# Kernel optimization log

Hardware: AMD Instinct MI355X
Metric: run time of the kernel (lower is better)

## Reference

```python
import jax, jax.numpy as jnp
import numpy as np

D_MODEL = 1024

def setup_inputs() -> dict:
    key = jax.random.key(0)
    ks = jax.random.split(key, 7)
    x = jax.random.normal(ks[0], (4, 2048, D_MODEL), dtype=jnp.float32)
    s = 1.0 / np.sqrt(D_MODEL)
    Wq = jax.random.uniform(ks[1], (D_MODEL, D_MODEL), jnp.float32, -s, s)
    bq = jax.random.uniform(ks[2], (D_MODEL,), jnp.float32, -s, s)
    Wk = jax.random.uniform(ks[3], (D_MODEL, D_MODEL), jnp.float32, -s, s)
    bk = jax.random.uniform(ks[4], (D_MODEL,), jnp.float32, -s, s)
    Wv = jax.random.uniform(ks[5], (D_MODEL, D_MODEL), jnp.float32, -s, s)
    bv = jax.random.uniform(ks[6], (D_MODEL,), jnp.float32, -s, s)
    return {"x": x, "Wq": Wq, "bq": bq, "Wk": Wk, "bk": bk, "Wv": Wv, "bv": bv}

def reference(x, Wq, bq, Wk, bk, Wv, bv):
    # x: [B, S, D]; Linear weights stored torch-style [out, in] -> y = x @ W.T + b
    B, S, D = x.shape
    q = jnp.einsum('bsd,ed->bse', x, Wq) + bq
    k = jnp.einsum('bsd,ed->bse', x, Wk) + bk
    v = jnp.einsum('bsd,ed->bse', x, Wv) + bv
    scores = jnp.einsum('bqd,bkd->bqk', q, k) / jnp.sqrt(jnp.float32(D))
    causal = jnp.tril(jnp.ones((S, S), dtype=bool))  # True = allowed
    scores = jnp.where(causal[None], scores, -jnp.inf)
    probs = jax.nn.softmax(scores, axis=-1)
    return jnp.einsum('bqk,bkd->bqd', probs, v)
```

## Files before the change

### kernel.cpp

```cpp
#include <hip/hip_runtime.h>
#include <hip/hip_bf16.h>
#include <stdint.h>
#include <math.h>

using bf16 = __hip_bfloat16;
typedef __bf16 bf16x8 __attribute__((ext_vector_type(8)));
typedef float  f32x4  __attribute__((ext_vector_type(4)));

#define AS1 __attribute__((address_space(1)))
#define AS3 __attribute__((address_space(3)))

__device__ __forceinline__ void async_cp16(const void* g, void* l) {
    __builtin_amdgcn_global_load_lds((const AS1 void*)g, (AS3 void*)l, 16, 0, 0);
}

__global__ __launch_bounds__(256, 2) void gemm_qkv(
    const bf16* __restrict__ xb,
    const bf16* __restrict__ Wqb, const bf16* __restrict__ Wkb, const bf16* __restrict__ Wvb,
    const float* __restrict__ bq, const float* __restrict__ bk, const float* __restrict__ bv,
    bf16* __restrict__ Qb, bf16* __restrict__ Kb, bf16* __restrict__ Vt)
{
    const int bn = blockIdx.x, bm = blockIdx.y;
    const int seg = bn >> 3, bn_loc = bn & 7;
    const bf16*  W    = seg == 0 ? Wqb : (seg == 1 ? Wkb : Wvb);
    const float* bias = seg == 0 ? bq  : (seg == 1 ? bk  : bv);

    __shared__ bf16 sA[128 * 64];
    __shared__ bf16 sB[128 * 64];

    const int tid  = threadIdx.x;
    const int wave = tid >> 6, lane = tid & 63;
    const int wm = (wave >> 1) * 64, wn = (wave & 1) * 64;
    const int quad = lane >> 4, r16 = lane & 15;

    const bf16* Ab = xb + (long)bm * 128 * 1024;
    const bf16* Bb = W  + (long)bn_loc * 128 * 1024;

    const int rl = lane >> 3;
    const int cb = (lane & 7) ^ rl;
    const bf16* gA = Ab + (long)(wave * 32 + rl) * 1024 + cb * 8;
    const bf16* gB = Bb + (long)(wave * 32 + rl) * 1024 + cb * 8;
    char* lA = (char*)sA + wave * 32 * 128;
    char* lB = (char*)sB + wave * 32 * 128;

    f32x4 acc[4][4];
    const f32x4 zero = {0.f, 0.f, 0.f, 0.f};
#pragma unroll
    for (int i = 0; i < 4; i++)
#pragma unroll
        for (int j = 0; j < 4; j++) acc[i][j] = zero;

    for (int k0 = 0; k0 < 1024; k0 += 64) {
#pragma unroll
        for (int c = 0; c < 4; c++) {
            async_cp16(gA + (long)c * 8 * 1024 + k0, lA + c * 1024);
            async_cp16(gB + (long)c * 8 * 1024 + k0, lB + c * 1024);
        }
        __syncthreads();
#pragma unroll
        for (int kk = 0; kk < 2; kk++) {
            bf16x8 af[4], bfr[4];
#pragma unroll
            for (int t = 0; t < 4; t++) {
                int row  = wm + t * 16 + r16;
                int slot = (kk * 4 + quad) ^ (row & 7);
                af[t] = *(const bf16x8*)((const char*)sA + row * 128 + slot * 16);
            }
#pragma unroll
            for (int t = 0; t < 4; t++) {
                int row  = wn + t * 16 + r16;
                int slot = (kk * 4 + quad) ^ (row & 7);
                bfr[t] = *(const bf16x8*)((const char*)sB + row * 128 + slot * 16);
            }
#pragma unroll
            for (int mt = 0; mt < 4; mt++)
#pragma unroll
                for (int nt = 0; nt < 4; nt++)
                    acc[mt][nt] = __builtin_amdgcn_mfma_f32_16x16x32_bf16(
                        af[mt], bfr[nt], acc[mt][nt], 0, 0, 0);
        }
        __syncthreads();
    }

    bf16* O = seg == 0 ? Qb : Kb;
#pragma unroll
    for (int mt = 0; mt < 4; mt++) {
#pragma unroll
        for (int nt = 0; nt < 4; nt++) {
            int col = bn_loc * 128 + wn + nt * 16 + r16;
            float badd = bias[col];
#pragma unroll
            for (int rg = 0; rg < 4; rg++) {
                long token = (long)bm * 128 + wm + mt * 16 + quad * 4 + rg;
                bf16 v = __float2bfloat16(acc[mt][nt][rg] + badd);
                if (seg < 2) O[token * 1024 + col] = v;
                else         Vt[(long)col * 8192 + token] = v;
            }
        }
    }
}

__global__ __launch_bounds__(256, 2) void gemm_scores(
    const bf16* __restrict__ Qb, const bf16* __restrict__ Kb,
    bf16* __restrict__ P, float* __restrict__ spart)
{
    const int t = blockIdx.x, bz = blockIdx.z;
    int bm = (int)((sqrtf(8.f * t + 1.f) - 1.f) * 0.5f);
    while ((bm + 1) * (bm + 2) / 2 <= t) bm++;
    while (bm * (bm + 1) / 2 > t) bm--;
    const int bn = t - bm * (bm + 1) / 2;
    const bool diag = (bn == bm);

    __shared__ bf16 sA[128 * 64];
    __shared__ bf16 sB[128 * 64];

    const int tid  = threadIdx.x;
    const int wave = tid >> 6, lane = tid & 63;
    const int wm = (wave >> 1) * 64, wn = (wave & 1) * 64;
    const int quad = lane >> 4, r16 = lane & 15;
    const int half = wave & 1;

    const bf16* Ab = Qb + (long)bz * 2048 * 1024 + (long)bm * 128 * 1024;
    const bf16* Bb = Kb + (long)bz * 2048 * 1024 + (long)bn * 128 * 1024;

    const int rl = lane >> 3;
    const int cb = (lane & 7) ^ rl;
    const bf16* gA = Ab + (long)(wave * 32 + rl) * 1024 + cb * 8;
    const bf16* gB = Bb + (long)(wave * 32 + rl) * 1024 + cb * 8;
    char* lA = (char*)sA + wave * 32 * 128;
    char* lB = (char*)sB + wave * 32 * 128;

    f32x4 acc[4][4];
    const f32x4 zero = {0.f, 0.f, 0.f, 0.f};
#pragma unroll
    for (int i = 0; i < 4; i++)
#pragma unroll
        for (int j = 0; j < 4; j++) acc[i][j] = zero;

    for (int k0 = 0; k0 < 1024; k0 += 64) {
#pragma unroll
        for (int c = 0; c < 4; c++) {
            async_cp16(gA + (long)c * 8 * 1024 + k0, lA + c * 1024);
            async_cp16(gB + (long)c * 8 * 1024 + k0, lB + c * 1024);
        }
        __syncthreads();
#pragma unroll
        for (int kk = 0; kk < 2; kk++) {
            bf16x8 af[4], bfr[4];
#pragma unroll
            for (int t2 = 0; t2 < 4; t2++) {
                int row  = wm + t2 * 16 + r16;
                int slot = (kk * 4 + quad) ^ (row & 7);
                af[t2] = *(const bf16x8*)((const char*)sA + row * 128 + slot * 16);
            }
#pragma unroll
            for (int t2 = 0; t2 < 4; t2++) {
                int row  = wn + t2 * 16 + r16;
                int slot = (kk * 4 + quad) ^ (row & 7);
                bfr[t2] = *(const bf16x8*)((const char*)sB + row * 128 + slot * 16);
            }
#pragma unroll
            for (int mt = 0; mt < 4; mt++)
#pragma unroll
                for (int nt = 0; nt < 4; nt++)
                    acc[mt][nt] = __builtin_amdgcn_mfma_f32_16x16x32_bf16(
                        af[mt], bfr[nt], acc[mt][nt], 0, 0, 0);
        }
        __syncthreads();
    }

    bf16* Pb = P + (long)bz * 2048 * 2048 + (long)bm * 128 * 2048 + bn * 128;
    float rowsum[4][4];
#pragma unroll
    for (int mt = 0; mt < 4; mt++)
#pragma unroll
        for (int rg = 0; rg < 4; rg++) rowsum[mt][rg] = 0.f;

#pragma unroll
    for (int mt = 0; mt < 4; mt++) {
#pragma unroll
        for (int nt = 0; nt < 4; nt++) {
            int rcol = wn + nt * 16 + r16;
#pragma unroll
            for (int rg = 0; rg < 4; rg++) {
                int rrow = wm + mt * 16 + quad * 4 + rg;
                float e = (diag && rcol > rrow)
                            ? 0.f : __expf(acc[mt][nt][rg] * 0.03125f);
                Pb[(long)rrow * 2048 + rcol] = __float2bfloat16(e);
                rowsum[mt][rg] += e;
            }
        }
    }
#pragma unroll
    for (int off = 1; off < 16; off <<= 1)
#pragma unroll
        for (int mt = 0; mt < 4; mt++)
#pragma unroll
            for (int rg = 0; rg < 4; rg++)
                rowsum[mt][rg] += __shfl_xor(rowsum[mt][rg], off);

    float* red = (float*)sA;
    if (r16 == 0) {
#pragma unroll
        for (int mt = 0; mt < 4; mt++)
#pragma unroll
            for (int rg = 0; rg < 4; rg++)
                red[half * 128 + wm + mt * 16 + quad * 4 + rg] = rowsum[mt][rg];
    }
    __syncthreads();
    if (tid < 128)
        spart[((long)bz * 16 + bn) * 2048 + bm * 128 + tid] = red[tid] + red[128 + tid];
}

__global__ __launch_bounds__(256, 2) void gemm_pv(
    const bf16* __restrict__ P, const bf16* __restrict__ Vt,
    const float* __restrict__ spart, float* __restrict__ out)
{
    const int bn = blockIdx.x, bm = 15 - blockIdx.y, bz = blockIdx.z;
    const int nb = bm + 1;

    __shared__ bf16 sA[128 * 64];
    __shared__ bf16 sB[128 * 64];
    __shared__ float invl[128];

    const int tid  = threadIdx.x;
    const int wave = tid >> 6, lane = tid & 63;
    const int wm = (wave >> 1) * 64, wn = (wave & 1) * 64;
    const int quad = lane >> 4, r16 = lane & 15;

    if (tid < 128) {
        long base = (long)bz * 16 * 2048 + (long)bm * 128 + tid;
        float l = 0.f;
        for (int j = 0; j < nb; j++) l += spart[base + j * 2048];
        invl[tid] = 1.f / l;
    }

    const bf16* Ab = P  + (long)bz * 2048 * 2048 + (long)bm * 128 * 2048;
    const bf16* Bb = Vt + (long)bz * 2048 + (long)bn * 128 * 8192;

    const int rl = lane >> 3;
    const int cb = (lane & 7) ^ rl;
    const bf16* gA = Ab + (long)(wave * 32 + rl) * 2048 + cb * 8;
    const bf16* gB = Bb + (long)(wave * 32 + rl) * 8192 + cb * 8;
    char* lA = (char*)sA + wave * 32 * 128;
    char* lB = (char*)sB + wave * 32 * 128;

    f32x4 acc[4][4];
    const f32x4 zero = {0.f, 0.f, 0.f, 0.f};
#pragma unroll
    for (int i = 0; i < 4; i++)
#pragma unroll
        for (int j = 0; j < 4; j++) acc[i][j] = zero;

    const int Keff = nb * 128;
    for (int k0 = 0; k0 < Keff; k0 += 64) {
#pragma unroll
        for (int c = 0; c < 4; c++) {
            async_cp16(gA + (long)c * 8 * 2048 + k0, lA + c * 1024);
            async_cp16(gB + (long)c * 8 * 8192 + k0, lB + c * 1024);
        }
        __syncthreads();
#pragma unroll
        for (int kk = 0; kk < 2; kk++) {
            bf16x8 af[4], bfr[4];
#pragma unroll
            for (int t = 0; t < 4; t++) {
                int row  = wm + t * 16 + r16;
                int slot = (kk * 4 + quad) ^ (row & 7);
                af[t] = *(const bf16x8*)((const char*)sA + row * 128 + slot * 16);
            }
#pragma unroll
            for (int t = 0; t < 4; t++) {
                int row  = wn + t * 16 + r16;
                int slot = (kk * 4 + quad) ^ (row & 7);
                bfr[t] = *(const bf16x8*)((const char*)sB + row * 128 + slot * 16);
            }
#pragma unroll
            for (int mt = 0; mt < 4; mt++)
#pragma unroll
                for (int nt = 0; nt < 4; nt++)
                    acc[mt][nt] = __builtin_amdgcn_mfma_f32_16x16x32_bf16(
                        af[mt], bfr[nt], acc[mt][nt], 0, 0, 0);
        }
        __syncthreads();
    }

    float* Ob = out + (long)bz * 2048 * 1024 + (long)bm * 128 * 1024 + bn * 128;
#pragma unroll
    for (int mt = 0; mt < 4; mt++) {
#pragma unroll
        for (int nt = 0; nt < 4; nt++) {
            int rcol = wn + nt * 16 + r16;
#pragma unroll
            for (int rg = 0; rg < 4; rg++) {
                int rrow = wm + mt * 16 + quad * 4 + rg;
                Ob[(long)rrow * 1024 + rcol] = acc[mt][nt][rg] * invl[rrow];
            }
        }
    }
}

__global__ __launch_bounds__(256) void cvt_all(
    const float* __restrict__ x,
    const float* __restrict__ Wq, const float* __restrict__ Wk, const float* __restrict__ Wv,
    bf16* __restrict__ xb, bf16* __restrict__ dq, bf16* __restrict__ dk, bf16* __restrict__ dv)
{
    int b = blockIdx.x;
    const float* s; bf16* d; long off;
    if (b < 8192) { s = x; d = xb; off = (long)b * 1024; }
    else {
        int w = (b - 8192) >> 10, lb = (b - 8192) & 1023;
        s = w == 0 ? Wq : (w == 1 ? Wk : Wv);
        d = w == 0 ? dq : (w == 1 ? dk : dv);
        off = (long)lb * 1024;
    }
    long i = off + threadIdx.x * 4;
    float4 v = *(const float4*)(s + i);
    union { ushort4 u; bf16 h[4]; } o;
    o.h[0] = __float2bfloat16(v.x);
    o.h[1] = __float2bfloat16(v.y);
    o.h[2] = __float2bfloat16(v.z);
    o.h[3] = __float2bfloat16(v.w);
    *(ushort4*)(d + i) = o.u;
}

extern "C" void kernel_launch(void* const* d_in, const int* in_sizes, int n_in,
                              void* d_out, int out_size, void* d_ws, size_t ws_size,
                              hipStream_t stream)
{
    (void)in_sizes; (void)n_in; (void)out_size; (void)ws_size;
    const float* x  = (const float*)d_in[0];
    const float* Wq = (const float*)d_in[1];
    const float* bq = (const float*)d_in[2];
    const float* Wk = (const float*)d_in[3];
    const float* bk = (const float*)d_in[4];
    const float* Wv = (const float*)d_in[5];
    const float* bv = (const float*)d_in[6];
    float* out = (float*)d_out;

    char* ws = (char*)d_ws;
    bf16* xb  = (bf16*)ws;  ws += (long)8192 * 1024 * 2;
    bf16* Wqb = (bf16*)ws;  ws += (long)1024 * 1024 * 2;
    bf16* Wkb = (bf16*)ws;  ws += (long)1024 * 1024 * 2;
    bf16* Wvb = (bf16*)ws;  ws += (long)1024 * 1024 * 2;
    bf16* Qb  = (bf16*)ws;  ws += (long)8192 * 1024 * 2;
    bf16* Kb  = (bf16*)ws;  ws += (long)8192 * 1024 * 2;
    bf16* Vt  = (bf16*)ws;  ws += (long)8192 * 1024 * 2;
    bf16* P   = (bf16*)ws;  ws += (long)4 * 2048 * 2048 * 2;
    float* spart = (float*)ws; ws += (long)4 * 16 * 2048 * 4;

    cvt_all<<<8192 + 3072, 256, 0, stream>>>(x, Wq, Wk, Wv, xb, Wqb, Wkb, Wvb);

    gemm_qkv<<<dim3(24, 64), 256, 0, stream>>>(
        xb, Wqb, Wkb, Wvb, bq, bk, bv, Qb, Kb, Vt);

    gemm_scores<<<dim3(136, 1, 4), 256, 0, stream>>>(Qb, Kb, P, spart);

    gemm_pv<<<dim3(8, 16, 4), 256, 0, stream>>>(P, Vt, spart, out);
}
```

Measured before the change: 253.8 us.

## Store Q/K as FP8 and compute attention scores with FP8 MFMA

Q and K projections are now quantized to FP8 (no scaling) in the QKV GEMM epilogue, and the scores GEMM loads byte tiles with K=128 per stage and uses the fp8 16x16x32 MFMA. This halves Q/K memory traffic and doubles MFMA throughput for the QK^T stage. The V transpose store is also vectorized into 4-element writes. It risks accuracy loss since FP8 without per-tensor scaling may not meet tolerance, and per-byte Q/K stores are uncoalesced.

After: 217.6 us. 1.17x faster.

```diff
diff --git a/kernel.cpp b/kernel.cpp
--- a/kernel.cpp
+++ b/kernel.cpp
@@ -1,24 +1,29 @@
 #include <hip/hip_runtime.h>
 #include <hip/hip_bf16.h>
 #include <stdint.h>
-#include <math.h>
 
 using bf16 = __hip_bfloat16;
 typedef __bf16 bf16x8 __attribute__((ext_vector_type(8)));
 typedef float  f32x4  __attribute__((ext_vector_type(4)));
+typedef long   i64;
+typedef unsigned char u8;
 
 #define AS1 __attribute__((address_space(1)))
 #define AS3 __attribute__((address_space(3)))
 
 __device__ __forceinline__ void async_cp16(const void* g, void* l) {
     __builtin_amdgcn_global_load_lds((const AS1 void*)g, (AS3 void*)l, 16, 0, 0);
+}
+
+__device__ __forceinline__ unsigned pk8_lo(float a, float b, unsigned old) {
+    return __builtin_amdgcn_cvt_pk_fp8_f32(a, b, old, false);
 }
 
 __global__ __launch_bounds__(256, 2) void gemm_qkv(
     const bf16* __restrict__ xb,
     const bf16* __restrict__ Wqb, const bf16* __restrict__ Wkb, const bf16* __restrict__ Wvb,
     const float* __restrict__ bq, const float* __restrict__ bk, const float* __restrict__ bv,
-    bf16* __restrict__ Qb, bf16* __restrict__ Kb, bf16* __restrict__ Vt)
+    u8* __restrict__ Qq, u8* __restrict__ Kq, bf16* __restrict__ Vt)
 {
     const int bn = blockIdx.x, bm = blockIdx.y;
     const int seg = bn >> 3, bn_loc = bn & 7;
@@ -82,26 +87,42 @@
         __syncthreads();
     }
 
-    bf16* O = seg == 0 ? Qb : Kb;
-#pragma unroll
-    for (int mt = 0; mt < 4; mt++) {
-#pragma unroll
-        for (int nt = 0; nt < 4; nt++) {
-            int col = bn_loc * 128 + wn + nt * 16 + r16;
-            float badd = bias[col];
-#pragma unroll
-            for (int rg = 0; rg < 4; rg++) {
-                long token = (long)bm * 128 + wm + mt * 16 + quad * 4 + rg;
-                bf16 v = __float2bfloat16(acc[mt][nt][rg] + badd);
-                if (seg < 2) O[token * 1024 + col] = v;
-                else         Vt[(long)col * 8192 + token] = v;
+    if (seg < 2) {
+        u8* O = seg == 0 ? Qq : Kq;
+#pragma unroll
+        for (int mt = 0; mt < 4; mt++) {
+#pragma unroll
+            for (int nt = 0; nt < 4; nt++) {
+                int col = bn_loc * 128 + wn + nt * 16 + r16;
+                float badd = bias[col];
+#pragma unroll
+                for (int rg = 0; rg < 4; rg++) {
+                    long token = (long)bm * 128 + wm + mt * 16 + quad * 4 + rg;
+                    float v = acc[mt][nt][rg] + badd;
+                    O[token * 1024 + col] = (u8)(pk8_lo(v, v, 0u) & 0xFF);
+                }
+            }
+        }
+    } else {
+#pragma unroll
+        for (int mt = 0; mt < 4; mt++) {
+#pragma unroll
+            for (int nt = 0; nt < 4; nt++) {
+                int col = bn_loc * 128 + wn + nt * 16 + r16;
+                float badd = bias[col];
+                long token0 = (long)bm * 128 + wm + mt * 16 + quad * 4;
+                union { ushort4 u; bf16 h[4]; } o;
+#pragma unroll
+                for (int rg = 0; rg < 4; rg++)
+                    o.h[rg] = __float2bfloat16(acc[mt][nt][rg] + badd);
+                *(ushort4*)&Vt[(long)col * 8192 + token0] = o.u;
             }
         }
     }
 }
 
 __global__ __launch_bounds__(256, 2) void gemm_scores(
-    const bf16* __restrict__ Qb, const bf16* __restrict__ Kb,
+    const u8* __restrict__ Qq, const u8* __restrict__ Kq,
     bf16* __restrict__ P, float* __restrict__ spart)
 {
     const int t = blockIdx.x, bz = blockIdx.z;
@@ -111,24 +132,24 @@
     const int bn = t - bm * (bm + 1) / 2;
     const bool diag = (bn == bm);
 
-    __shared__ bf16 sA[128 * 64];
-    __shared__ bf16 sB[128 * 64];
+    __shared__ u8 sA[128 * 128];
+    __shared__ u8 sB[128 * 128];
 
     const int tid  = threadIdx.x;
     const int wave = tid >> 6, lane = tid & 63;
     const int wm = (wave >> 1) * 64, wn = (wave & 1) * 64;
     const int quad = lane >> 4, r16 = lane & 15;
-    const int half = wave & 1;
-
-    const bf16* Ab = Qb + (long)bz * 2048 * 1024 + (long)bm * 128 * 1024;
-    const bf16* Bb = Kb + (long)bz * 2048 * 1024 + (long)bn * 128 * 1024;
+    const int whalf = wave & 1;
+
+    const u8* Ab = Qq + (long)bz * 2048 * 1024 + (long)bm * 128 * 1024;
+    const u8* Bb = Kq + (long)bz * 2048 * 1024 + (long)bn * 128 * 1024;
 
     const int rl = lane >> 3;
     const int cb = (lane & 7) ^ rl;
-    const bf16* gA = Ab + (long)(wave * 32 + rl) * 1024 + cb * 8;
-    const bf16* gB = Bb + (long)(wave * 32 + rl) * 1024 + cb * 8;
-    char* lA = (char*)sA + wave * 32 * 128;
-    char* lB = (char*)sB + wave * 32 * 128;
+    const u8* gA = Ab + (long)(wave * 32 + rl) * 1024 + cb * 16;
+    const u8* gB = Bb + (long)(wave * 32 + rl) * 1024 + cb * 16;
+    u8* lA = sA + wave * 32 * 128;
+    u8* lB = sB + wave * 32 * 128;
 
     f32x4 acc[4][4];
     const f32x4 zero = {0.f, 0.f, 0.f, 0.f};
@@ -137,7 +158,8 @@
 #pragma unroll
         for (int j = 0; j < 4; j++) acc[i][j] = zero;
 
-    for (int k0 = 0; k0 < 1024; k0 += 64) {
+    for (int it = 0; it < 8; ++it) {
+        const int k0 = it * 128;
 #pragma unroll
         for (int c = 0; c < 4; c++) {
             async_cp16(gA + (long)c * 8 * 1024 + k0, lA + c * 1024);
@@ -145,26 +167,28 @@
         }
         __syncthreads();
 #pragma unroll
-        for (int kk = 0; kk < 2; kk++) {
-            bf16x8 af[4], bfr[4];
+        for (int kk = 0; kk < 4; kk++) {
+            const int g  = kk * 2 + (quad >> 1);
+            const int hb = (quad & 1) * 8;
+            i64 av[4], bv[4];
 #pragma unroll
             for (int t2 = 0; t2 < 4; t2++) {
                 int row  = wm + t2 * 16 + r16;
-                int slot = (kk * 4 + quad) ^ (row & 7);
-                af[t2] = *(const bf16x8*)((const char*)sA + row * 128 + slot * 16);
+                int slot = g ^ (row & 7);
+                av[t2] = *(const i64*)(sA + row * 128 + slot * 16 + hb);
             }
 #pragma unroll
             for (int t2 = 0; t2 < 4; t2++) {
                 int row  = wn + t2 * 16 + r16;
-                int slot = (kk * 4 + quad) ^ (row & 7);
-                bfr[t2] = *(const bf16x8*)((const char*)sB + row * 128 + slot * 16);
+                int slot = g ^ (row & 7);
+                bv[t2] = *(const i64*)(sB + row * 128 + slot * 16 + hb);
             }
 #pragma unroll
             for (int mt = 0; mt < 4; mt++)
 #pragma unroll
                 for (int nt = 0; nt < 4; nt++)
-                    acc[mt][nt] = __builtin_amdgcn_mfma_f32_16x16x32_bf16(
-                        af[mt], bfr[nt], acc[mt][nt], 0, 0, 0);
+                    acc[mt][nt] = __builtin_amdgcn_mfma_f32_16x16x32_fp8_fp8(
+                        av[mt], bv[nt], acc[mt][nt], 0, 0, 0);
         }
         __syncthreads();
     }
@@ -205,7 +229,7 @@
         for (int mt = 0; mt < 4; mt++)
 #pragma unroll
             for (int rg = 0; rg < 4; rg++)
-                red[half * 128 + wm + mt * 16 + quad * 4 + rg] = rowsum[mt][rg];
+                red[whalf * 128 + wm + mt * 16 + quad * 4 + rg] = rowsum[mt][rg];
     }
     __syncthreads();
     if (tid < 128)
@@ -343,8 +367,8 @@
     bf16* Wqb = (bf16*)ws;  ws += (long)1024 * 1024 * 2;
     bf16* Wkb = (bf16*)ws;  ws += (long)1024 * 1024 * 2;
     bf16* Wvb = (bf16*)ws;  ws += (long)1024 * 1024 * 2;
-    bf16* Qb  = (bf16*)ws;  ws += (long)8192 * 1024 * 2;
-    bf16* Kb  = (bf16*)ws;  ws += (long)8192 * 1024 * 2;
+    u8*  Qq   = (u8*)ws;    ws += (long)8192 * 1024;
+    u8*  Kq   = (u8*)ws;    ws += (long)8192 * 1024;
     bf16* Vt  = (bf16*)ws;  ws += (long)8192 * 1024 * 2;
     bf16* P   = (bf16*)ws;  ws += (long)4 * 2048 * 2048 * 2;
     float* spart = (float*)ws; ws += (long)4 * 16 * 2048 * 4;
@@ -352,9 +376,9 @@
     cvt_all<<<8192 + 3072, 256, 0, stream>>>(x, Wq, Wk, Wv, xb, Wqb, Wkb, Wvb);
 
     gemm_qkv<<<dim3(24, 64), 256, 0, stream>>>(
-        xb, Wqb, Wkb, Wvb, bq, bk, bv, Qb, Kb, Vt);
-
-    gemm_scores<<<dim3(136, 1, 4), 256, 0, stream>>>(Qb, Kb, P, spart);
+        xb, Wqb, Wkb, Wvb, bq, bk, bv, Qq, Kq, Vt);
+
+    gemm_scores<<<dim3(136, 1, 4), 256, 0, stream>>>(Qq, Kq, P, spart);
 
     gemm_pv<<<dim3(8, 16, 4), 256, 0, stream>>>(P, Vt, spart, out);
 }
```
